# Performance work log

Hardware: AMD Instinct MI355X
Metric: run time of the kernel (lower is better)

The kernel has to match this reference:

```python
import jax, jax.numpy as jnp
import numpy as np

IMG_W = 224
STRIDE = 16
NUM_HEADS = 12
# 196 grid centers, x-major order: [(x, y) for x in ... for y in ...]
_xs = np.arange(STRIDE // 2, IMG_W, STRIDE)
GRIDS = jnp.asarray(np.array([(x, y) for x in _xs for y in _xs], dtype=np.float32))  # [196, 2]


def setup_inputs() -> dict:
    key = jax.random.key(0)
    ks = jax.random.split(key, 8)
    B, N, C = 256, 198, 768
    s = 0.02
    return {
        "x": jax.random.normal(ks[0], (B, N, C), dtype=jnp.float32),
        "w_qkv": jax.random.normal(ks[1], (C, 3 * C), dtype=jnp.float32) * s,  # qkv_bias=False
        "w_proj": jax.random.normal(ks[2], (C, C), dtype=jnp.float32) * s,
        "b_proj": jax.random.normal(ks[3], (C,), dtype=jnp.float32) * s,
        "w_D": jax.random.normal(ks[4], (C, 3), dtype=jnp.float32) * s,
        "b_D": jax.random.normal(ks[5], (3,), dtype=jnp.float32) * s,
        "w_cen": jax.random.normal(ks[6], (C, 6), dtype=jnp.float32) * s,
        "b_cen": jax.random.normal(ks[7], (6,), dtype=jnp.float32) * s,
    }


def reference(x, w_qkv, w_proj, b_proj, w_D, b_D, w_cen, b_cen):
    B, N, C = x.shape
    H = NUM_HEADS
    dh = C // H
    scale = dh ** (-0.5)

    qkv = (x @ w_qkv).reshape(B, N, 3, H, dh).transpose(2, 0, 3, 1, 4)  # [3,B,H,N,dh]
    q, k, v = qkv[0], qkv[1], qkv[2]

    attn = jnp.einsum('bhnd,bhmd->bhnm', q, k) * scale
    attn = jax.nn.softmax(attn, axis=-1)  # [B,H,N,N]

    # CLS-token query, heads concatenated: q.permute(2,0,1,3).reshape(N,B,C)[0]
    q0 = q[:, :, 0, :].reshape(B, C)
    D = IMG_W * jax.nn.sigmoid(q0 @ w_D + b_D)                      # [B,3]
    cen = jax.nn.sigmoid((q0 @ w_cen + b_cen).reshape(B, 3, 2))     # [B,3,2]

    # mixture-of-gaussian blobs over 196 patch grid positions
    sigma = (D / 2.0)[..., None]                                    # [B,3,1]
    coord = cen * (IMG_W - 1)                                       # [B,3,2]
    dist = ((coord[:, :, None, :] - GRIDS[None, None]) ** 2).sum(-1)  # [B,3,196]
    mgb = jnp.exp(-dist / (2.0 * sigma ** 2)) / 2.0 / 3.14 / sigma ** 2
    mgb = mgb / mgb.sum(-1, keepdims=True)
    mgb = mgb.sum(axis=1) / 3.0                                     # [B,196]
    mgb = jnp.concatenate([jnp.ones((B, 2), mgb.dtype), mgb], axis=1)  # [B,N]

    # head-score reweighting of the CLS attention row
    hs = attn[:, :, 0, :].transpose(1, 0, 2)   # [H,B,N] == permute(1,2,0,3) squeezed
    hs = hs * mgb[None]                        # broadcast over heads
    hs = hs / hs.sum(-1, keepdims=True)
    # replicate torch masked_scatter flat-order semantics:
    # source flattened in (h,b,n) order is written into target positions in (b,h,n) order
    new_row = hs.reshape(-1).reshape(B, H, N)
    attn = attn.at[:, :, 0, :].set(new_row)

    out = jnp.einsum('bhnm,bhmd->bhnd', attn, v)      # [B,H,N,dh]
    out = out.transpose(0, 2, 1, 3).reshape(B, N, C)
    out = out @ w_proj + b_proj
    return cen, attn[:, :, 0, :], out
```

## Files before the change

### kernel.cpp

```cpp
#include <hip/hip_runtime.h>
#include <cstdint>
#include <cstddef>

typedef __attribute__((ext_vector_type(4))) float  f32x4;
typedef __attribute__((ext_vector_type(8))) __bf16 bf16x8;
typedef __attribute__((ext_vector_type(4))) __bf16 bf16x4;

#define MFMA16(A, B, C) __builtin_amdgcn_mfma_f32_16x16x32_bf16((A), (B), (C), 0, 0, 0)

#define GLOAD_LDS16(gp, lp)                                        \
    __builtin_amdgcn_global_load_lds(                              \
        (const __attribute__((address_space(1))) void*)(gp),       \
        (__attribute__((address_space(3))) void*)(lp), 16, 0, 0)

#define NB 256
#define NN 198
#define NC 768
#define NH 12

__global__ __launch_bounds__(256) void cast_to_bf16(const float* __restrict__ in,
                                                    __bf16* __restrict__ out, int n8) {
    int i = blockIdx.x * 256 + threadIdx.x;
    if (i < n8) {
        const float4 f0 = reinterpret_cast<const float4*>(in)[i * 2];
        const float4 f1 = reinterpret_cast<const float4*>(in)[i * 2 + 1];
        bf16x8 h;
        h[0] = (__bf16)f0.x; h[1] = (__bf16)f0.y; h[2] = (__bf16)f0.z; h[3] = (__bf16)f0.w;
        h[4] = (__bf16)f1.x; h[5] = (__bf16)f1.y; h[6] = (__bf16)f1.z; h[7] = (__bf16)f1.w;
        reinterpret_cast<bf16x8*>(out)[i] = h;
    }
}

__global__ void transpose_to_bf16(const float* __restrict__ in, __bf16* __restrict__ out,
                                  int R, int Cc) {
    int idx = blockIdx.x * 256 + threadIdx.x;
    if (idx < R * Cc) {
        int r = idx / Cc, c = idx % Cc;
        out[(size_t)c * R + r] = (__bf16)in[idx];
    }
}

__global__ __launch_bounds__(512, 2) void gemm_qkv_v5(
    const __bf16* __restrict__ xb, const __bf16* __restrict__ wT,
    __bf16* __restrict__ qb, __bf16* __restrict__ kb, __bf16* __restrict__ vb,
    float* __restrict__ q0) {
    __shared__ __bf16 As[2][256 * 64];
    __shared__ __bf16 Bs[2][256 * 64];
    const int bid = blockIdx.x;
    const int xcd = bid & 7, lin = bid >> 3;
    const int wgid = (xcd < 6 ? xcd * 223 : 6 * 223 + (xcd - 6) * 222) + lin;
    const int brow = (wgid / 9) * 256;
    const int bcol = (wgid % 9) * 256;
    const int tid = threadIdx.x, lane = tid & 63, wid = tid >> 6;
    const int wr = wid >> 2, wc = wid & 3;
    const int lr = lane & 15, lg = lane >> 4;

    const int srow = tid >> 3;
    const int sslot = (tid & 7) ^ ((tid >> 3) & 7);
    const __bf16* aSrc = xb + (size_t)(brow + srow) * 768 + sslot * 8;
    const __bf16* bSrc = wT + (size_t)(bcol + srow) * 768 + sslot * 8;
    const int key = lr & 7;

    f32x4 acc[8][4] = {};

#define STAGE5(buf, kk0)                                                       \
    {                                                                          \
        __bf16* aD = &As[buf][wid * 512];                                      \
        __bf16* bD = &Bs[buf][wid * 512];                                      \
        _Pragma("unroll")                                                      \
        for (int j = 0; j < 4; ++j) {                                          \
            GLOAD_LDS16(aSrc + (size_t)j * 64 * 768 + (kk0), aD + j * 4096);   \
            GLOAD_LDS16(bSrc + (size_t)j * 64 * 768 + (kk0), bD + j * 4096);   \
        }                                                                      \
    }

#define COMPUTE5(buf)                                                          \
    {                                                                          \
        const __bf16* Ab = As[buf];                                            \
        const __bf16* Bb = Bs[buf];                                            \
        bf16x8 bfr[2][4];                                                      \
        _Pragma("unroll")                                                      \
        for (int kk = 0; kk < 2; ++kk)                                         \
            _Pragma("unroll")                                                  \
            for (int nt = 0; nt < 4; ++nt)                                     \
                bfr[kk][nt] = *reinterpret_cast<const bf16x8*>(                \
                    Bb + (wc * 64 + nt * 16 + lr) * 64 +                       \
                    (((kk * 4 + lg) ^ key) * 8));                              \
        __builtin_amdgcn_s_setprio(1);                                         \
        _Pragma("unroll")                                                      \
        for (int mt = 0; mt < 8; ++mt) {                                       \
            const int arow = (wr * 128 + mt * 16 + lr) * 64;                   \
            bf16x8 a0 = *reinterpret_cast<const bf16x8*>(                      \
                Ab + arow + ((lg ^ key) * 8));                                 \
            bf16x8 a1 = *reinterpret_cast<const bf16x8*>(                      \
                Ab + arow + (((4 + lg) ^ key) * 8));                           \
            _Pragma("unroll")                                                  \
            for (int nt = 0; nt < 4; ++nt)                                     \
                acc[mt][nt] = MFMA16(a0, bfr[0][nt], acc[mt][nt]);             \
            _Pragma("unroll")                                                  \
            for (int nt = 0; nt < 4; ++nt)                                     \
                acc[mt][nt] = MFMA16(a1, bfr[1][nt], acc[mt][nt]);             \
        }                                                                      \
        __builtin_amdgcn_s_setprio(0);                                         \
    }

    STAGE5(0, 0);
    STAGE5(1, 64);
    for (int tau = 0; tau < 12; ++tau) {
        if (tau == 11) asm volatile("s_waitcnt vmcnt(0)" ::: "memory");
        else           asm volatile("s_waitcnt vmcnt(8)" ::: "memory");
        __builtin_amdgcn_s_barrier();
        __builtin_amdgcn_sched_barrier(0);
        COMPUTE5(tau & 1);
        __builtin_amdgcn_sched_barrier(0);
        __builtin_amdgcn_s_barrier();
        __builtin_amdgcn_sched_barrier(0);
        if (tau < 10) STAGE5(tau & 1, (tau + 2) * 64);
    }
#undef STAGE5
#undef COMPUTE5

#pragma unroll
    for (int mt = 0; mt < 8; ++mt) {
        int grow0 = brow + wr * 128 + mt * 16 + lg * 4;
#pragma unroll
        for (int nt = 0; nt < 4; ++nt) {
            int gcol = bcol + wc * 64 + nt * 16 + lr;
            int sidx = gcol / 768;
            int rem  = gcol % 768;
            __bf16* dstbuf = (sidx == 0) ? qb : (sidx == 1) ? kb : vb;
            int hh = rem >> 6, dd = rem & 63;
#pragma unroll
            for (int r = 0; r < 4; ++r) {
                int grow = grow0 + r;
                int bb = grow / 198, nn2 = grow % 198;
                float val = acc[mt][nt][r];
                dstbuf[(((size_t)bb * 12 + hh) * 198 + nn2) * 64 + dd] = (__bf16)val;
                if (sidx == 0 && nn2 == 0) q0[bb * 768 + rem] = val;
            }
        }
    }
}

__global__ __launch_bounds__(256) void mgb_kernel(
    const float* __restrict__ q0, const float* __restrict__ wD,
    const float* __restrict__ bD, const float* __restrict__ wcen,
    const float* __restrict__ bcen, float* __restrict__ cen_out,
    float* __restrict__ mgb) {
    const int b = blockIdx.x, t = threadIdx.x;
    __shared__ float qs[768];
    __shared__ float red[256];
    __shared__ float vals[9];
    qs[t]       = q0[b * 768 + t];
    qs[t + 256] = q0[b * 768 + t + 256];
    qs[t + 512] = q0[b * 768 + t + 512];
    __syncthreads();
    for (int j = 0; j < 9; ++j) {
        float p;
        if (j < 3)
            p = qs[t] * wD[t * 3 + j] + qs[t + 256] * wD[(t + 256) * 3 + j] +
                qs[t + 512] * wD[(t + 512) * 3 + j];
        else {
            int c = j - 3;
            p = qs[t] * wcen[t * 6 + c] + qs[t + 256] * wcen[(t + 256) * 6 + c] +
                qs[t + 512] * wcen[(t + 512) * 6 + c];
        }
        red[t] = p;
        __syncthreads();
        for (int off = 128; off > 0; off >>= 1) {
            if (t < off) red[t] += red[t + off];
            __syncthreads();
        }
        if (t == 0) {
            float bias = (j < 3) ? bD[j] : bcen[j - 3];
            vals[j] = 1.f / (1.f + __expf(-(red[0] + bias)));
        }
        __syncthreads();
    }
    if (t < 6) cen_out[b * 6 + t] = vals[3 + t];

    float e3[3] = {0.f, 0.f, 0.f};
    if (t < 196) {
        float gx = 8.f + 16.f * (float)(t / 14);
        float gy = 8.f + 16.f * (float)(t % 14);
#pragma unroll
        for (int j = 0; j < 3; ++j) {
            float sig = 112.f * vals[j];
            float cx = vals[3 + 2 * j] * 223.f;
            float cy = vals[3 + 2 * j + 1] * 223.f;
            float dx = cx - gx, dy = cy - gy;
            e3[j] = __expf(-(dx * dx + dy * dy) / (2.f * sig * sig));
        }
    }
    float js[3];
    for (int j = 0; j < 3; ++j) {
        red[t] = e3[j];
        __syncthreads();
        for (int off = 128; off > 0; off >>= 1) {
            if (t < off) red[t] += red[t + off];
            __syncthreads();
        }
        js[j] = red[0];
        __syncthreads();
    }
    if (t < 196) {
        float m = (e3[0] / js[0] + e3[1] / js[1] + e3[2] / js[2]) * (1.f / 3.f);
        mgb[(size_t)b * 198 + 2 + t] = m;
    }
    if (t < 2) mgb[(size_t)b * 198 + t] = 1.f;
}

__global__ __launch_bounds__(256) void attn_kernel(
    const __bf16* __restrict__ qb, const __bf16* __restrict__ kb,
    const __bf16* __restrict__ vb, float* __restrict__ p0,
    __bf16* __restrict__ outp) {
    __shared__ __bf16 Vt[64][216];
    __shared__ __bf16 Plds[4][16][216];
    const int bh = blockIdx.x;
    const int b = bh / 12, h = bh % 12;
    const __bf16* Qp = qb + (size_t)bh * NN * 64;
    const __bf16* Kp = kb + (size_t)bh * NN * 64;
    const __bf16* Vp = vb + (size_t)bh * NN * 64;
    const int tid = threadIdx.x, lane = tid & 63, wid = tid >> 6;
    const int lr = lane & 15, lg = lane >> 4;

    for (int i = tid; i < 208 * 8; i += 256) {
        int key = i >> 3, d0 = (i & 7) << 3;
        int krow = key < 198 ? key : 197;
        bf16x8 hv = *reinterpret_cast<const bf16x8*>(Vp + krow * 64 + d0);
#pragma unroll
        for (int j = 0; j < 8; ++j) Vt[d0 + j][key] = hv[j];
    }
    __syncthreads();

    for (int ch = wid; ch < 13; ch += 4) {
        int n0 = ch * 16;
        int qrow = n0 + lr; if (qrow > 197) qrow = 197;
        bf16x8 qf0 = *reinterpret_cast<const bf16x8*>(Qp + qrow * 64 + lg * 8);
        bf16x8 qf1 = *reinterpret_cast<const bf16x8*>(Qp + qrow * 64 + 32 + lg * 8);
        f32x4 sa[13];
#pragma unroll
        for (int t2 = 0; t2 < 13; ++t2) {
            int krow = t2 * 16 + lr; if (krow > 197) krow = 197;
            bf16x8 kf0 = *reinterpret_cast<const bf16x8*>(Kp + krow * 64 + lg * 8);
            bf16x8 kf1 = *reinterpret_cast<const bf16x8*>(Kp + krow * 64 + 32 + lg * 8);
            f32x4 a = (f32x4){0.f, 0.f, 0.f, 0.f};
            a = MFMA16(kf0, qf0, a);
            a = MFMA16(kf1, qf1, a);
            sa[t2] = a;
        }
        float rmax = -1e30f;
#pragma unroll
        for (int t2 = 0; t2 < 13; ++t2)
#pragma unroll
            for (int r = 0; r < 4; ++r) {
                int key = t2 * 16 + lg * 4 + r;
                float vv = (key < 198) ? sa[t2][r] * 0.125f : -1e30f;
                sa[t2][r] = vv;
                rmax = fmaxf(rmax, vv);
            }
        rmax = fmaxf(rmax, __shfl_xor(rmax, 16));
        rmax = fmaxf(rmax, __shfl_xor(rmax, 32));
        float rsum = 0.f;
#pragma unroll
        for (int t2 = 0; t2 < 13; ++t2)
#pragma unroll
            for (int r = 0; r < 4; ++r) {
                float e = __expf(sa[t2][r] - rmax);
                sa[t2][r] = e;
                rsum += e;
            }
        rsum += __shfl_xor(rsum, 16);
        rsum += __shfl_xor(rsum, 32);
        float inv = 1.f / rsum;

        if (ch == 0 && lr == 0) {
#pragma unroll
            for (int t2 = 0; t2 < 13; ++t2)
#pragma unroll
                for (int r = 0; r < 4; ++r) {
                    int key = t2 * 16 + lg * 4 + r;
                    if (key < 198) p0[(size_t)bh * 198 + key] = sa[t2][r] * inv;
                }
        }
#pragma unroll
        for (int t2 = 0; t2 < 13; ++t2) {
            bf16x4 pk;
#pragma unroll
            for (int r = 0; r < 4; ++r) pk[r] = (__bf16)(sa[t2][r] * inv);
            *reinterpret_cast<bf16x4*>(&Plds[wid][lr][t2 * 16 + lg * 4]) = pk;
        }
        asm volatile("s_waitcnt lgkmcnt(0)" ::: "memory");

        f32x4 o[4];
#pragma unroll
        for (int mt = 0; mt < 4; ++mt) o[mt] = (f32x4){0.f, 0.f, 0.f, 0.f};
#pragma unroll
        for (int ks = 0; ks < 7; ++ks) {
            int kbase = ks * 32 + lg * 8;
            bf16x8 pf;
            if (kbase < 208)
                pf = *reinterpret_cast<const bf16x8*>(&Plds[wid][lr][kbase]);
            else {
#pragma unroll
                for (int j = 0; j < 8; ++j) pf[j] = (__bf16)0.f;
            }
#pragma unroll
            for (int mt = 0; mt < 4; ++mt) {
                bf16x8 vf;
                if (kbase < 208)
                    vf = *reinterpret_cast<const bf16x8*>(&Vt[mt * 16 + lr][kbase]);
                else {
#pragma unroll
                    for (int j = 0; j < 8; ++j) vf[j] = (__bf16)0.f;
                }
                o[mt] = MFMA16(vf, pf, o[mt]);
            }
        }
        int qg = n0 + lr;
        if (qg < 198) {
            __bf16* dst = outp + ((size_t)b * 198 + qg) * 768 + h * 64;
#pragma unroll
            for (int mt = 0; mt < 4; ++mt) {
                bf16x4 pk;
#pragma unroll
                for (int r = 0; r < 4; ++r) pk[r] = (__bf16)o[mt][r];
                *reinterpret_cast<bf16x4*>(dst + mt * 16 + lg * 4) = pk;
            }
        }
    }
}

__global__ __launch_bounds__(64) void reweight_kernel(
    const float* __restrict__ p0, const float* __restrict__ mgb,
    const __bf16* __restrict__ vb, float* __restrict__ attn_out,
    __bf16* __restrict__ outp) {
    const int t = blockIdx.x;
    const int b = t / 12, h = t % 12;
    const int h2 = t >> 8, b2 = t & 255;
    const int lane = threadIdx.x;
    __shared__ float nr[198];
    const float* pr = p0 + (size_t)(b2 * 12 + h2) * 198;
    const float* mr = mgb + (size_t)b2 * 198;
    float w[4];
    float ssum = 0.f;
#pragma unroll
    for (int i = 0; i < 4; ++i) {
        int n = lane + 64 * i;
        float xv = (n < 198) ? pr[n] * mr[n] : 0.f;
        w[i] = xv;
        ssum += xv;
    }
#pragma unroll
    for (int m = 1; m < 64; m <<= 1) ssum += __shfl_xor(ssum, m);
    float inv = 1.f / ssum;
#pragma unroll
    for (int i = 0; i < 4; ++i) {
        int n = lane + 64 * i;
        if (n < 198) {
            float xv = w[i] * inv;
            nr[n] = xv;
            attn_out[(size_t)t * 198 + n] = xv;
        }
    }
    __syncthreads();
    const __bf16* vp = vb + (size_t)t * 198 * 64;
    float acc = 0.f;
    for (int n = 0; n < 198; ++n) acc += nr[n] * (float)vp[n * 64 + lane];
    outp[((size_t)b * 198) * 768 + h * 64 + lane] = (__bf16)acc;
}

__global__ __launch_bounds__(512, 2) void gemm_proj_v5(
    const __bf16* __restrict__ A, const __bf16* __restrict__ wT,
    const float* __restrict__ bias, float* __restrict__ out) {
    __shared__ __bf16 As[2][256 * 64];
    __shared__ __bf16 Bs[2][256 * 64];
    const int bid = blockIdx.x;
    const int xcd = bid & 7, lin = bid >> 3;
    const int wgid = (xcd < 2 ? xcd * 75 : 2 * 75 + (xcd - 2) * 74) + lin;
    const int brow = (wgid / 3) * 256;
    const int bcol = (wgid % 3) * 256;
    const int tid = threadIdx.x, lane = tid & 63, wid = tid >> 6;
    const int wr = wid >> 2, wc = wid & 3;
    const int lr = lane & 15, lg = lane >> 4;

    const int srow = tid >> 3;
    const int sslot = (tid & 7) ^ ((tid >> 3) & 7);
    const __bf16* aSrc = A  + (size_t)(brow + srow) * 768 + sslot * 8;
    const __bf16* bSrc = wT + (size_t)(bcol + srow) * 768 + sslot * 8;
    const int key = lr & 7;

    f32x4 acc[8][4] = {};

#define STAGE6(buf, kk0)                                                       \
    {                                                                          \
        __bf16* aD = &As[buf][wid * 512];                                      \
        __bf16* bD = &Bs[buf][wid * 512];                                      \
        _Pragma("unroll")                                                      \
        for (int j = 0; j < 4; ++j) {                                          \
            GLOAD_LDS16(aSrc + (size_t)j * 64 * 768 + (kk0), aD + j * 4096);   \
            GLOAD_LDS16(bSrc + (size_t)j * 64 * 768 + (kk0), bD + j * 4096);   \
        }                                                                      \
    }

#define COMPUTE6(buf)                                                          \
    {                                                                          \
        const __bf16* Ab = As[buf];                                            \
        const __bf16* Bb = Bs[buf];                                            \
        bf16x8 bfr[2][4];                                                      \
        _Pragma("unroll")                                                      \
        for (int kk = 0; kk < 2; ++kk)                                         \
            _Pragma("unroll")                                                  \
            for (int nt = 0; nt < 4; ++nt)                                     \
                bfr[kk][nt] = *reinterpret_cast<const bf16x8*>(                \
                    Bb + (wc * 64 + nt * 16 + lr) * 64 +                       \
                    (((kk * 4 + lg) ^ key) * 8));                              \
        __builtin_amdgcn_s_setprio(1);                                         \
        _Pragma("unroll")                                                      \
        for (int mt = 0; mt < 8; ++mt) {                                       \
            const int arow = (wr * 128 + mt * 16 + lr) * 64;                   \
            bf16x8 a0 = *reinterpret_cast<const bf16x8*>(                      \
                Ab + arow + ((lg ^ key) * 8));                                 \
            bf16x8 a1 = *reinterpret_cast<const bf16x8*>(                      \
                Ab + arow + (((4 + lg) ^ key) * 8));                           \
            _Pragma("unroll")                                                  \
            for (int nt = 0; nt < 4; ++nt)                                     \
                acc[mt][nt] = MFMA16(a0, bfr[0][nt], acc[mt][nt]);             \
            _Pragma("unroll")                                                  \
            for (int nt = 0; nt < 4; ++nt)                                     \
                acc[mt][nt] = MFMA16(a1, bfr[1][nt], acc[mt][nt]);             \
        }                                                                      \
        __builtin_amdgcn_s_setprio(0);                                         \
    }

    STAGE6(0, 0);
    STAGE6(1, 64);
    for (int tau = 0; tau < 12; ++tau) {
        if (tau == 11) asm volatile("s_waitcnt vmcnt(0)" ::: "memory");
        else           asm volatile("s_waitcnt vmcnt(8)" ::: "memory");
        __builtin_amdgcn_s_barrier();
        __builtin_amdgcn_sched_barrier(0);
        COMPUTE6(tau & 1);
        __builtin_amdgcn_sched_barrier(0);
        __builtin_amdgcn_s_barrier();
        __builtin_amdgcn_sched_barrier(0);
        if (tau < 10) STAGE6(tau & 1, (tau + 2) * 64);
    }
#undef STAGE6
#undef COMPUTE6

#pragma unroll
    for (int mt = 0; mt < 8; ++mt) {
#pragma unroll
        for (int nt = 0; nt < 4; ++nt) {
            int gcol = bcol + wc * 64 + nt * 16 + lr;
            float bv = bias[gcol];
#pragma unroll
            for (int r = 0; r < 4; ++r) {
                int grow = brow + wr * 128 + mt * 16 + lg * 4 + r;
                out[(size_t)grow * 768 + gcol] = acc[mt][nt][r] + bv;
            }
        }
    }
}

extern "C" void kernel_launch(void* const* d_in, const int* in_sizes, int n_in,
                              void* d_out, int out_size, void* d_ws, size_t ws_size,
                              hipStream_t stream) {
    const float* x      = (const float*)d_in[0];
    const float* w_qkv  = (const float*)d_in[1];
    const float* w_proj = (const float*)d_in[2];
    const float* b_proj = (const float*)d_in[3];
    const float* w_D    = (const float*)d_in[4];
    const float* b_D    = (const float*)d_in[5];
    const float* w_cen  = (const float*)d_in[6];
    const float* b_cen  = (const float*)d_in[7];

    float* out      = (float*)d_out;
    float* cen_out  = out;
    float* attn_out = out + 1536;
    float* proj_out = out + 1536 + 608256;

    char* ws = (char*)d_ws;
    size_t off = 0;
    auto carve = [&](size_t bytes) {
        void* p = ws + off;
        off += (bytes + 255) & ~(size_t)255;
        return p;
    };
    __bf16* wqkvT  = (__bf16*)carve((size_t)2304 * 768 * 2);
    __bf16* wprojT = (__bf16*)carve((size_t)768 * 768 * 2);
    __bf16* qb     = (__bf16*)carve((size_t)3072 * 198 * 64 * 2);
    __bf16* kb     = (__bf16*)carve((size_t)3072 * 198 * 64 * 2);
    __bf16* vb     = (__bf16*)carve((size_t)3072 * 198 * 64 * 2);
    __bf16* outp   = (__bf16*)carve((size_t)50688 * 768 * 2);
    float*  q0     = (float*)carve((size_t)256 * 768 * 4);
    float*  mgb    = (float*)carve((size_t)256 * 198 * 4);
    float*  p0     = (float*)carve((size_t)3072 * 198 * 4);

    __bf16* xb = outp;

    cast_to_bf16<<<(50688 * 768 / 8 + 255) / 256, 256, 0, stream>>>(x, xb, 50688 * 768 / 8);
    transpose_to_bf16<<<(768 * 2304 + 255) / 256, 256, 0, stream>>>(w_qkv, wqkvT, 768, 2304);
    transpose_to_bf16<<<(768 * 768 + 255) / 256, 256, 0, stream>>>(w_proj, wprojT, 768, 768);
    gemm_qkv_v5<<<1782, 512, 0, stream>>>(xb, wqkvT, qb, kb, vb, q0);
    mgb_kernel<<<256, 256, 0, stream>>>(q0, w_D, b_D, w_cen, b_cen, cen_out, mgb);
    attn_kernel<<<3072, 256, 0, stream>>>(qb, kb, vb, p0, outp);
    reweight_kernel<<<3072, 64, 0, stream>>>(p0, mgb, vb, attn_out, outp);
    gemm_proj_v5<<<594, 512, 0, stream>>>(outp, wprojT, b_proj, proj_out);
}
```

Baseline: 576.3 us.

## Software-pipeline GEMM LDS fragment loads, tile weight transpose, pack V transpose

Both GEMM main loops now load A fragments from LDS two M-tiles ahead in register ping-pong sets, with explicit lgkmcnt waits, so LDS reads overlap MFMA work. The last MFMA phase is moved after the barrier and next-stage global loads, hiding the prefetch issue behind compute. The weight transpose now goes through a 32x32 shared-memory tile to get coalesced reads and writes. The attention V transpose writes two keys at once as packed 32-bit stores. The register ping-pong raises VGPR pressure under a 2-blocks-per-CU bound, which risks spills.

```diff
diff --git a/kernel.cpp b/kernel.cpp
--- a/kernel.cpp
+++ b/kernel.cpp
@@ -31,16 +31,23 @@
     }
 }
 
-__global__ void transpose_to_bf16(const float* __restrict__ in, __bf16* __restrict__ out,
-                                  int R, int Cc) {
-    int idx = blockIdx.x * 256 + threadIdx.x;
-    if (idx < R * Cc) {
-        int r = idx / Cc, c = idx % Cc;
-        out[(size_t)c * R + r] = (__bf16)in[idx];
-    }
-}
-
-__global__ __launch_bounds__(512, 2) void gemm_qkv_v5(
+__global__ __launch_bounds__(256) void transpose_to_bf16(
+    const float* __restrict__ in, __bf16* __restrict__ out, int R, int Cc) {
+    __shared__ __bf16 tile[32][33];
+    const int ntc = Cc >> 5;
+    const int tc = blockIdx.x % ntc, tr = blockIdx.x / ntc;
+    const int c0 = tc * 32, r0 = tr * 32;
+    const int lx = threadIdx.x & 31, ly = threadIdx.x >> 5;
+#pragma unroll
+    for (int j = 0; j < 4; ++j)
+        tile[ly + j * 8][lx] = (__bf16)in[(size_t)(r0 + ly + j * 8) * Cc + c0 + lx];
+    __syncthreads();
+#pragma unroll
+    for (int j = 0; j < 4; ++j)
+        out[(size_t)(c0 + ly + j * 8) * R + r0 + lx] = tile[lx][ly + j * 8];
+}
+
+__global__ __launch_bounds__(512, 2) void gemm_qkv_v7(
     const __bf16* __restrict__ xb, const __bf16* __restrict__ wT,
     __bf16* __restrict__ qb, __bf16* __restrict__ kb, __bf16* __restrict__ vb,
     float* __restrict__ q0) {
@@ -63,7 +70,7 @@
 
     f32x4 acc[8][4] = {};
 
-#define STAGE5(buf, kk0)                                                       \
+#define STAGE7(buf, kk0)                                                       \
     {                                                                          \
         __bf16* aD = &As[buf][wid * 512];                                      \
         __bf16* bD = &Bs[buf][wid * 512];                                      \
@@ -74,51 +81,67 @@
         }                                                                      \
     }
 
-#define COMPUTE5(buf)                                                          \
-    {                                                                          \
-        const __bf16* Ab = As[buf];                                            \
-        const __bf16* Bb = Bs[buf];                                            \
-        bf16x8 bfr[2][4];                                                      \
-        _Pragma("unroll")                                                      \
-        for (int kk = 0; kk < 2; ++kk)                                         \
-            _Pragma("unroll")                                                  \
-            for (int nt = 0; nt < 4; ++nt)                                     \
-                bfr[kk][nt] = *reinterpret_cast<const bf16x8*>(                \
-                    Bb + (wc * 64 + nt * 16 + lr) * 64 +                       \
-                    (((kk * 4 + lg) ^ key) * 8));                              \
-        __builtin_amdgcn_s_setprio(1);                                         \
-        _Pragma("unroll")                                                      \
-        for (int mt = 0; mt < 8; ++mt) {                                       \
-            const int arow = (wr * 128 + mt * 16 + lr) * 64;                   \
-            bf16x8 a0 = *reinterpret_cast<const bf16x8*>(                      \
-                Ab + arow + ((lg ^ key) * 8));                                 \
-            bf16x8 a1 = *reinterpret_cast<const bf16x8*>(                      \
-                Ab + arow + (((4 + lg) ^ key) * 8));                           \
-            _Pragma("unroll")                                                  \
-            for (int nt = 0; nt < 4; ++nt)                                     \
-                acc[mt][nt] = MFMA16(a0, bfr[0][nt], acc[mt][nt]);             \
-            _Pragma("unroll")                                                  \
-            for (int nt = 0; nt < 4; ++nt)                                     \
-                acc[mt][nt] = MFMA16(a1, bfr[1][nt], acc[mt][nt]);             \
-        }                                                                      \
-        __builtin_amdgcn_s_setprio(0);                                         \
-    }
-
-    STAGE5(0, 0);
-    STAGE5(1, 64);
+#define LDA7(f0, f1, f2, f3, m0)                                               \
+    f0 = *reinterpret_cast<const bf16x8*>(                                     \
+        Ab + (wr * 128 + (m0) * 16 + lr) * 64 + ((lg ^ key) * 8));             \
+    f1 = *reinterpret_cast<const bf16x8*>(                                     \
+        Ab + (wr * 128 + (m0) * 16 + lr) * 64 + (((4 + lg) ^ key) * 8));       \
+    f2 = *reinterpret_cast<const bf16x8*>(                                     \
+        Ab + (wr * 128 + (m0) * 16 + 16 + lr) * 64 + ((lg ^ key) * 8));        \
+    f3 = *reinterpret_cast<const bf16x8*>(                                     \
+        Ab + (wr * 128 + (m0) * 16 + 16 + lr) * 64 + (((4 + lg) ^ key) * 8));
+
+#define MFMA_PHASE7(f0, f1, f2, f3, m0)                                        \
+    __builtin_amdgcn_s_setprio(1);                                             \
+    _Pragma("unroll")                                                          \
+    for (int nt = 0; nt < 4; ++nt) acc[(m0)][nt]     = MFMA16(f0, bfr[0][nt], acc[(m0)][nt]);     \
+    _Pragma("unroll")                                                          \
+    for (int nt = 0; nt < 4; ++nt) acc[(m0)][nt]     = MFMA16(f1, bfr[1][nt], acc[(m0)][nt]);     \
+    _Pragma("unroll")                                                          \
+    for (int nt = 0; nt < 4; ++nt) acc[(m0) + 1][nt] = MFMA16(f2, bfr[0][nt], acc[(m0) + 1][nt]); \
+    _Pragma("unroll")                                                          \
+    for (int nt = 0; nt < 4; ++nt) acc[(m0) + 1][nt] = MFMA16(f3, bfr[1][nt], acc[(m0) + 1][nt]); \
+    __builtin_amdgcn_s_setprio(0);
+
+    STAGE7(0, 0);
+    STAGE7(1, 64);
     for (int tau = 0; tau < 12; ++tau) {
+        const int b = tau & 1;
         if (tau == 11) asm volatile("s_waitcnt vmcnt(0)" ::: "memory");
         else           asm volatile("s_waitcnt vmcnt(8)" ::: "memory");
         __builtin_amdgcn_s_barrier();
         __builtin_amdgcn_sched_barrier(0);
-        COMPUTE5(tau & 1);
+        const __bf16* Ab = As[b];
+        const __bf16* Bb = Bs[b];
+        bf16x8 bfr[2][4];
+#pragma unroll
+        for (int kk = 0; kk < 2; ++kk)
+#pragma unroll
+            for (int nt = 0; nt < 4; ++nt)
+                bfr[kk][nt] = *reinterpret_cast<const bf16x8*>(
+                    Bb + (wc * 64 + nt * 16 + lr) * 64 + (((kk * 4 + lg) ^ key) * 8));
+        bf16x8 a0, a1, a2, a3, b0, b1, b2, b3;
+        LDA7(a0, a1, a2, a3, 0);
+        LDA7(b0, b1, b2, b3, 2);
+        asm volatile("s_waitcnt lgkmcnt(4)" ::: "memory");
+        __builtin_amdgcn_sched_barrier(0);
+        MFMA_PHASE7(a0, a1, a2, a3, 0);
+        LDA7(a0, a1, a2, a3, 4);
+        asm volatile("s_waitcnt lgkmcnt(4)" ::: "memory");
+        __builtin_amdgcn_sched_barrier(0);
+        MFMA_PHASE7(b0, b1, b2, b3, 2);
+        LDA7(b0, b1, b2, b3, 6);
+        asm volatile("s_waitcnt lgkmcnt(4)" ::: "memory");
+        __builtin_amdgcn_sched_barrier(0);
+        MFMA_PHASE7(a0, a1, a2, a3, 4);
+        asm volatile("s_waitcnt lgkmcnt(0)" ::: "memory");
         __builtin_amdgcn_sched_barrier(0);
         __builtin_amdgcn_s_barrier();
         __builtin_amdgcn_sched_barrier(0);
-        if (tau < 10) STAGE5(tau & 1, (tau + 2) * 64);
-    }
-#undef STAGE5
-#undef COMPUTE5
+        if (tau < 10) STAGE7(b, (tau + 2) * 64);
+        MFMA_PHASE7(b0, b1, b2, b3, 6);
+    }
+#undef STAGE7
 
 #pragma unroll
     for (int mt = 0; mt < 8; ++mt) {
@@ -224,12 +247,18 @@
     const int tid = threadIdx.x, lane = tid & 63, wid = tid >> 6;
     const int lr = lane & 15, lg = lane >> 4;
 
-    for (int i = tid; i < 208 * 8; i += 256) {
-        int key = i >> 3, d0 = (i & 7) << 3;
-        int krow = key < 198 ? key : 197;
-        bf16x8 hv = *reinterpret_cast<const bf16x8*>(Vp + krow * 64 + d0);
-#pragma unroll
-        for (int j = 0; j < 8; ++j) Vt[d0 + j][key] = hv[j];
+    for (int i = tid; i < 104 * 8; i += 256) {
+        int key2 = (i >> 3) * 2, d0 = (i & 7) << 3;
+        int kr0 = key2 < 198 ? key2 : 197;
+        int kr1 = key2 + 1 < 198 ? key2 + 1 : 197;
+        bf16x8 h0 = *reinterpret_cast<const bf16x8*>(Vp + kr0 * 64 + d0);
+        bf16x8 h1 = *reinterpret_cast<const bf16x8*>(Vp + kr1 * 64 + d0);
+#pragma unroll
+        for (int j = 0; j < 8; ++j) {
+            union { __bf16 hh[2]; unsigned u; } pk;
+            pk.hh[0] = h0[j]; pk.hh[1] = h1[j];
+            *reinterpret_cast<unsigned*>(&Vt[d0 + j][key2]) = pk.u;
+        }
     }
     __syncthreads();
 
@@ -370,7 +399,7 @@
     outp[((size_t)b * 198) * 768 + h * 64 + lane] = (__bf16)acc;
 }
 
-__global__ __launch_bounds__(512, 2) void gemm_proj_v5(
+__global__ __launch_bounds__(512, 2) void gemm_proj_v7(
     const __bf16* __restrict__ A, const __bf16* __restrict__ wT,
     const float* __restrict__ bias, float* __restrict__ out) {
     __shared__ __bf16 As[2][256 * 64];
@@ -392,7 +421,7 @@
 
     f32x4 acc[8][4] = {};
 
-#define STAGE6(buf, kk0)                                                       \
+#define STAGE8(buf, kk0)                                                       \
     {                                                                          \
         __bf16* aD = &As[buf][wid * 512];                                      \
         __bf16* bD = &Bs[buf][wid * 512];                                      \
@@ -403,51 +432,45 @@
         }                                                                      \
     }
 
-#define COMPUTE6(buf)                                                          \
-    {                                                                          \
-        const __bf16* Ab = As[buf];                                            \
-        const __bf16* Bb = Bs[buf];                                            \
-        bf16x8 bfr[2][4];                                                      \
-        _Pragma("unroll")                                                      \
-        for (int kk = 0; kk < 2; ++kk)                                         \
-            _Pragma("unroll")                                                  \
-            for (int nt = 0; nt < 4; ++nt)                                     \
-                bfr[kk][nt] = *reinterpret_cast<const bf16x8*>(                \
-                    Bb + (wc * 64 + nt * 16 + lr) * 64 +                       \
-                    (((kk * 4 + lg) ^ key) * 8));                              \
-        __builtin_amdgcn_s_setprio(1);                                         \
-        _Pragma("unroll")                                                      \
-        for (int mt = 0; mt < 8; ++mt) {                                       \
-            const int arow = (wr * 128 + mt * 16 + lr) * 64;                   \
-            bf16x8 a0 = *reinterpret_cast<const bf16x8*>(                      \
-                Ab + arow + ((lg ^ key) * 8));                                 \
-            bf16x8 a1 = *reinterpret_cast<const bf16x8*>(                      \
-                Ab + arow + (((4 + lg) ^ key) * 8));                           \
-            _Pragma("unroll")                                                  \
-            for (int nt = 0; nt < 4; ++nt)                                     \
-                acc[mt][nt] = MFMA16(a0, bfr[0][nt], acc[mt][nt]);             \
-            _Pragma("unroll")                                                  \
-            for (int nt = 0; nt < 4; ++nt)                                     \
-                acc[mt][nt] = MFMA16(a1, bfr[1][nt], acc[mt][nt]);             \
-        }                                                                      \
-        __builtin_amdgcn_s_setprio(0);                                         \
-    }
-
-    STAGE6(0, 0);
-    STAGE6(1, 64);
+    STAGE8(0, 0);
+    STAGE8(1, 64);
     for (int tau = 0; tau < 12; ++tau) {
+        const int b = tau & 1;
         if (tau == 11) asm volatile("s_waitcnt vmcnt(0)" ::: "memory");
         else           asm volatile("s_waitcnt vmcnt(8)" ::: "memory");
         __builtin_amdgcn_s_barrier();
         __builtin_amdgcn_sched_barrier(0);
-        COMPUTE6(tau & 1);
+        const __bf16* Ab = As[b];
+        const __bf16* Bb = Bs[b];
+        bf16x8 bfr[2][4];
+#pragma unroll
+        for (int kk = 0; kk < 2; ++kk)
+#pragma unroll
+            for (int nt = 0; nt < 4; ++nt)
+                bfr[kk][nt] = *reinterpret_cast<const bf16x8*>(
+                    Bb + (wc * 64 + nt * 16 + lr) * 64 + (((kk * 4 + lg) ^ key) * 8));
+        bf16x8 a0, a1, a2, a3, b0, b1, b2, b3;
+        LDA7(a0, a1, a2, a3, 0);
+        LDA7(b0, b1, b2, b3, 2);
+        asm volatile("s_waitcnt lgkmcnt(4)" ::: "memory");
+        __builtin_amdgcn_sched_barrier(0);
+        MFMA_PHASE7(a0, a1, a2, a3, 0);
+        LDA7(a0, a1, a2, a3, 4);
+        asm volatile("s_waitcnt lgkmcnt(4)" ::: "memory");
+        __builtin_amdgcn_sched_barrier(0);
+        MFMA_PHASE7(b0, b1, b2, b3, 2);
+        LDA7(b0, b1, b2, b3, 6);
+        asm volatile("s_waitcnt lgkmcnt(4)" ::: "memory");
+        __builtin_amdgcn_sched_barrier(0);
+        MFMA_PHASE7(a0, a1, a2, a3, 4);
+        asm volatile("s_waitcnt lgkmcnt(0)" ::: "memory");
         __builtin_amdgcn_sched_barrier(0);
         __builtin_amdgcn_s_barrier();
         __builtin_amdgcn_sched_barrier(0);
-        if (tau < 10) STAGE6(tau & 1, (tau + 2) * 64);
-    }
-#undef STAGE6
-#undef COMPUTE6
+        if (tau < 10) STAGE8(b, (tau + 2) * 64);
+        MFMA_PHASE7(b0, b1, b2, b3, 6);
+    }
+#undef STAGE8
 
 #pragma unroll
     for (int mt = 0; mt < 8; ++mt) {
@@ -501,11 +524,11 @@
     __bf16* xb = outp;
 
     cast_to_bf16<<<(50688 * 768 / 8 + 255) / 256, 256, 0, stream>>>(x, xb, 50688 * 768 / 8);
-    transpose_to_bf16<<<(768 * 2304 + 255) / 256, 256, 0, stream>>>(w_qkv, wqkvT, 768, 2304);
-    transpose_to_bf16<<<(768 * 768 + 255) / 256, 256, 0, stream>>>(w_proj, wprojT, 768, 768);
-    gemm_qkv_v5<<<1782, 512, 0, stream>>>(xb, wqkvT, qb, kb, vb, q0);
+    transpose_to_bf16<<<(2304 / 32) * (768 / 32), 256, 0, stream>>>(w_qkv, wqkvT, 768, 2304);
+    transpose_to_bf16<<<(768 / 32) * (768 / 32), 256, 0, stream>>>(w_proj, wprojT, 768, 768);
+    gemm_qkv_v7<<<1782, 512, 0, stream>>>(xb, wqkvT, qb, kb, vb, q0);
     mgb_kernel<<<256, 256, 0, stream>>>(q0, w_D, b_D, w_cen, b_cen, cen_out, mgb);
     attn_kernel<<<3072, 256, 0, stream>>>(qb, kb, vb, p0, outp);
     reweight_kernel<<<3072, 64, 0, stream>>>(p0, mgb, vb, attn_out, outp);
-    gemm_proj_v5<<<594, 512, 0, stream>>>(outp, wprojT, b_proj, proj_out);
-}
+    gemm_proj_v7<<<594, 512, 0, stream>>>(outp, wprojT, b_proj, proj_out);
+}
```

Result: faster. 524.0 us (-9.1%).
